# Kernel optimization log

Hardware: AMD Instinct MI355X
Metric: run time of the kernel (lower is better)

The kernel has to match this reference:

```python
import jax, jax.numpy as jnp
import numpy as np

B, L, DIM, H = 2, 2048, 2048, 16
D = DIM // H  # head_dim = 128
EPS = 1e-6


def _rope_freqs(seq_len: int, head_dim: int, theta: float = 10000.0) -> jnp.ndarray:
    # Flux-style rotation matrix: [1, 1, L, D/2, 2, 2]
    pos = np.arange(seq_len, dtype=np.float32)
    inv = 1.0 / (theta ** (np.arange(0, head_dim, 2, dtype=np.float32) / head_dim))
    ang = np.einsum('l,d->ld', pos, inv)  # [L, D/2]
    cos, sin = np.cos(ang), np.sin(ang)
    rot = np.stack([np.stack([cos, -sin], -1), np.stack([sin, cos], -1)], -2)  # [L, D/2, 2, 2]
    return jnp.asarray(rot[None, None])


def _rms_norm(x, scale):
    rrms = jax.lax.rsqrt(jnp.mean(jnp.square(x), axis=-1, keepdims=True) + EPS)
    return x * rrms * scale


def _apply_rope(xq, xk, freqs_cis):
    # xq/xk: [B, H, L, D]; freqs_cis: [1, 1, L, D/2, 2, 2]
    def rot(x):
        xr = x.reshape(*x.shape[:-1], -1, 1, 2)  # [B,H,L,D/2,1,2]
        out = freqs_cis[..., 0] * xr[..., 0] + freqs_cis[..., 1] * xr[..., 1]
        return out.reshape(x.shape)
    return rot(xq), rot(xk)


def setup_inputs() -> dict:
    key = jax.random.key(0)
    ks = jax.random.split(key, 4)
    x = jax.random.normal(ks[0], (B, L, DIM), dtype=jnp.float32)
    qkv_w = jax.random.normal(ks[1], (DIM, 3 * DIM), dtype=jnp.float32) * 0.02
    qkv_b = jnp.zeros((3 * DIM,), dtype=jnp.float32)
    q_scale = jnp.ones((D,), dtype=jnp.float32)
    k_scale = jnp.ones((D,), dtype=jnp.float32)
    proj_w = jax.random.normal(ks[2], (DIM, DIM), dtype=jnp.float32) * 0.02
    proj_b = jnp.zeros((DIM,), dtype=jnp.float32)
    pe = _rope_freqs(L, D)
    return {"x": x, "pe": pe, "qkv_w": qkv_w, "qkv_b": qkv_b,
            "q_scale": q_scale, "k_scale": k_scale,
            "proj_w": proj_w, "proj_b": proj_b}


def reference(x, pe, qkv_w, qkv_b, q_scale, k_scale, proj_w, proj_b):
    b, l, _ = x.shape
    qkv = x @ qkv_w + qkv_b                      # [B, L, 3*DIM]
    qkv = qkv.reshape(b, l, 3, H, D)
    qkv = jnp.transpose(qkv, (2, 0, 3, 1, 4))    # [3, B, H, L, D]
    q, k, v = qkv[0], qkv[1], qkv[2]
    q = _rms_norm(q, q_scale)
    k = _rms_norm(k, k_scale)
    q, k = _apply_rope(q, k, pe)
    scores = jnp.einsum('bhqd,bhkd->bhqk', q, k) / jnp.sqrt(jnp.float32(D))
    attn = jax.nn.softmax(scores, axis=-1)
    o = jnp.einsum('bhqk,bhkd->bhqd', attn, v)   # [B, H, L, D]
    o = jnp.transpose(o, (0, 2, 1, 3)).reshape(b, l, H * D)
    return o @ proj_w + proj_b
```

## Files before the change

kernel.cpp:

```cpp
#include <hip/hip_runtime.h>
#include <cstdint>
#include <cstddef>

#define BB 2
#define HB 16
#define LL 2048
#define DD 128
#define MM 4096
#define KK 2048
#define N1 6144
#define N2 2048
#define BHLD (BB*HB*LL*DD)

typedef unsigned short u16;
typedef __bf16 bf16x8 __attribute__((ext_vector_type(8)));
typedef short  s16x4  __attribute__((ext_vector_type(4)));
typedef float  f32x4  __attribute__((ext_vector_type(4)));

typedef __attribute__((address_space(1))) void* as1_ptr;
typedef __attribute__((address_space(3))) void* as3_ptr;

__device__ __forceinline__ void gload16(const void* g, void* l) {
  __builtin_amdgcn_global_load_lds((as1_ptr)g, (as3_ptr)l, 16, 0, 0);
}

__device__ __forceinline__ float bf2f(u16 u) {
  union { unsigned v; float f; } c; c.v = ((unsigned)u) << 16; return c.f;
}
__device__ __forceinline__ u16 f2bf(float f) {
  unsigned u = __builtin_bit_cast(unsigned, f);
  return (u16)((u + 0x7FFFu + ((u >> 16) & 1u)) >> 16);
}


__global__ __launch_bounds__(256) void f32_to_bf16_vec(
    const float* __restrict__ in, u16* __restrict__ out, int n4) {
  int i = blockIdx.x * 256 + threadIdx.x;
  if (i >= n4) return;
  float4 v = ((const float4*)in)[i];
  ushort4 o;
  o.x = f2bf(v.x); o.y = f2bf(v.y); o.z = f2bf(v.z); o.w = f2bf(v.w);
  ((ushort4*)out)[i] = o;
}

__global__ __launch_bounds__(256) void transpose_f32_bf16(
    const float* __restrict__ in, u16* __restrict__ out, int R, int C) {
  __shared__ float t[32][33];
  int c0 = blockIdx.x * 32, r0 = blockIdx.y * 32;
  int tx = threadIdx.x & 31, ty = threadIdx.x >> 5;
#pragma unroll
  for (int i = ty; i < 32; i += 8)
    t[i][tx] = in[(size_t)(r0 + i) * C + c0 + tx];
  __syncthreads();
#pragma unroll
  for (int i = ty; i < 32; i += 8)
    out[(size_t)(c0 + i) * R + r0 + tx] = f2bf(t[tx][i]);
}

template<int MODE>
__global__ __launch_bounds__(256, 4) void gemm_bt(
    const u16* __restrict__ A, const u16* __restrict__ Bt,
    const float* __restrict__ bias, void* __restrict__ Cout,
    const float* __restrict__ pe, const float* __restrict__ qsc,
    const float* __restrict__ ksc,
    int Msz, int Nsz, int Ksz)
{
  __shared__ __align__(16) u16 As[128*64];
  __shared__ __align__(16) u16 Bs[128*64];
  const int tid  = threadIdx.x;
  const int lane = tid & 63;
  const int wid  = tid >> 6;
  const int l15  = lane & 15, quad = lane >> 4;
  const int m0 = blockIdx.y * 128, n0 = blockIdx.x * 128;
  const int wm = (wid >> 1) * 64, wn = (wid & 1) * 64;

  f32x4 acc[4][4] = {};

  for (int ks = 0; ks < Ksz; ks += 64) {
    __syncthreads();
#pragma unroll
    for (int j = 0; j < 4; j++) {
      const int s = (wid*4 + j)*64 + lane;
      const int row = s >> 3, pc = (s & 7) ^ (row & 7);
      gload16(&A [(size_t)(m0 + row) * Ksz + ks + pc*8], &As[(wid*4 + j)*512]);
      gload16(&Bt[(size_t)(n0 + row) * Ksz + ks + pc*8], &Bs[(wid*4 + j)*512]);
    }
    __syncthreads();
#pragma unroll
    for (int kh = 0; kh < 2; kh++) {
      bf16x8 af[4], bfr[4];
#pragma unroll
      for (int i = 0; i < 4; i++) {
        const int r = wm + i*16 + l15;
        af[i]  = *(const bf16x8*)&As[r*64 + (((kh*4 + quad) ^ (r & 7)))*8];
      }
#pragma unroll
      for (int i = 0; i < 4; i++) {
        const int r = wn + i*16 + l15;
        bfr[i] = *(const bf16x8*)&Bs[r*64 + (((kh*4 + quad) ^ (r & 7)))*8];
      }
#pragma unroll
      for (int i = 0; i < 4; i++)
#pragma unroll
        for (int j = 0; j < 4; j++)
          acc[i][j] = __builtin_amdgcn_mfma_f32_16x16x32_bf16(af[i], bfr[j], acc[i][j], 0, 0, 0);
    }
  }

  if (MODE == 0) {
    u16* qkvp = (u16*)Cout;
    const int t = n0 >> 11;
    const int hh = (n0 & 2047) >> 7;
#pragma unroll
    for (int i = 0; i < 4; i++)
#pragma unroll
      for (int j = 0; j < 4; j++) {
        const float bv = bias[n0 + wn + j*16 + l15];
#pragma unroll
        for (int r = 0; r < 4; r++) acc[i][j][r] += bv;
      }

    if (t == 2) {
#pragma unroll
      for (int i = 0; i < 4; i++)
#pragma unroll
        for (int j = 0; j < 4; j++) {
          const int d = wn + j*16 + l15;
#pragma unroll
          for (int r = 0; r < 4; r++) {
            const int row = m0 + wm + i*16 + quad*4 + r;
            const int b = row >> 11, l = row & (LL - 1);
            qkvp[(size_t)2 * BHLD + (((size_t)(b*HB + hh)) * DD + d) * LL + l] =
                f2bf(acc[i][j][r]);
          }
        }
    } else {
      float (*red)[2] = (float (*)[2])As;
      const float* sc = (t == 0) ? qsc : ksc;
      __syncthreads();
#pragma unroll
      for (int i = 0; i < 4; i++)
#pragma unroll
        for (int r = 0; r < 4; r++) {
          float s2 = 0.f;
#pragma unroll
          for (int j = 0; j < 4; j++) { const float v = acc[i][j][r]; s2 += v * v; }
#pragma unroll
          for (int m = 1; m < 16; m <<= 1) s2 += __shfl_xor(s2, m, 64);
          if (l15 == 0) red[wm + i*16 + quad*4 + r][wid & 1] = s2;
        }
      __syncthreads();
#pragma unroll
      for (int i = 0; i < 4; i++)
#pragma unroll
        for (int r = 0; r < 4; r++) {
          const int rowl = wm + i*16 + quad*4 + r;
          const float tot = red[rowl][0] + red[rowl][1];
          float rr = rsqrtf(tot * (1.0f/128.0f) + 1e-6f);
          if (t == 0) rr *= 0.08838834764831845f;
          const int row = m0 + rowl, b = row >> 11, l = row & (LL - 1);
#pragma unroll
          for (int j = 0; j < 4; j++) {
            const int d = wn + j*16 + l15;
            const float y = acc[i][j][r] * rr * sc[d];
            const float p = __shfl_xor(y, 1, 64);
            const float2 pp = *(const float2*)&pe[(size_t)l * 256 + (d >> 1) * 4 + (d & 1) * 2];
            const float o = pp.x * ((d & 1) ? p : y) + pp.y * ((d & 1) ? y : p);
            qkvp[(size_t)t * BHLD + (((size_t)(b*HB + hh)) * LL + l) * DD + d] = f2bf(o);
          }
        }
    }
  } else {
#pragma unroll
    for (int i = 0; i < 4; i++)
#pragma unroll
      for (int j = 0; j < 4; j++) {
        const int col = n0 + wn + j*16 + l15;
        const float bv = bias[col];
#pragma unroll
        for (int r = 0; r < 4; r++) {
          const int row = m0 + wm + i*16 + quad*4 + r;
          ((float*)Cout)[(size_t)row * Nsz + col] = acc[i][j][r] + bv;
        }
      }
  }
}

#define BKT 64
__global__ __launch_bounds__(256, 2) void attn(
    const u16* __restrict__ qkv, u16* __restrict__ Oout)
{
  __shared__ __align__(16) u16 Ksh[2][BKT * DD];
  __shared__ __align__(16) u16 Vsh[2][DD * BKT];

  const int bh = blockIdx.x >> 4, qt = blockIdx.x & 15;
  const int wid = threadIdx.x >> 6, lane = threadIdx.x & 63;
  const int l15 = lane & 15, quad = lane >> 4;
  const int q0 = qt * 128 + wid * 32;
  const u16* qp = qkv + (size_t)bh * LL * DD;
  const u16* kp = qkv + (size_t)BHLD + (size_t)bh * LL * DD;
  const u16* vp = qkv + (size_t)2 * BHLD + (size_t)bh * DD * LL;

  bf16x8 qb[2][4];
#pragma unroll
  for (int qf = 0; qf < 2; qf++)
#pragma unroll
    for (int f = 0; f < 4; f++)
      qb[qf][f] = *(const bf16x8*)&qp[(size_t)(q0 + qf*16 + l15) * DD + f*32 + quad*8];

  float l_acc[2] = {0.f, 0.f};
  f32x4 oacc[2][8] = {};

  auto stage = [&](int buf, int k0) {
#pragma unroll
    for (int j = 0; j < 4; j++) {
      const int s = (wid*4 + j)*64 + lane;
      {
        const int r = s >> 4, c = s & 15;
        const int lc = (c & 8) | ((c & 7) ^ (r & 7));
        gload16(&kp[(size_t)(k0 + r) * DD + lc*8], &Ksh[buf][(wid*4 + j)*512]);
      }
      {
        const int r = s >> 3, c = s & 7;
        const int lc = c ^ (r & 7);
        gload16(&vp[(size_t)r * LL + k0 + lc*8], &Vsh[buf][(wid*4 + j)*512]);
      }
    }
  };

  stage(0, 0);
  int cur = 0;

  for (int k0 = 0; k0 < LL; k0 += BKT) {
    __syncthreads();
    if (k0 + BKT < LL) stage(cur ^ 1, k0 + BKT);

    f32x4 s[2][4] = {};
#pragma unroll
    for (int f = 0; f < 4; f++) {
      bf16x8 kf[4];
#pragma unroll
      for (int mt = 0; mt < 4; mt++) {
        const int rr = mt*16 + l15;
        const int Lc = f*4 + quad;
        const int pc = (Lc & 8) | ((Lc & 7) ^ (rr & 7));
        kf[mt] = *(const bf16x8*)&Ksh[cur][rr*DD + pc*8];
      }
      __builtin_amdgcn_s_setprio(1);
#pragma unroll
      for (int qf = 0; qf < 2; qf++)
#pragma unroll
        for (int mt = 0; mt < 4; mt++)
          s[qf][mt] = __builtin_amdgcn_mfma_f32_16x16x32_bf16(kf[mt], qb[qf][f], s[qf][mt], 0, 0, 0);
      __builtin_amdgcn_s_setprio(0);
    }

    s16x4 pa[2][4];
#pragma unroll
    for (int qf = 0; qf < 2; qf++) {
#pragma unroll
      for (int mt = 0; mt < 4; mt++) {
        float p0 = __expf(s[qf][mt][0] - 12.f);
        float p1 = __expf(s[qf][mt][1] - 12.f);
        float p2 = __expf(s[qf][mt][2] - 12.f);
        float p3 = __expf(s[qf][mt][3] - 12.f);
        l_acc[qf] += (p0 + p1) + (p2 + p3);
        pa[qf][mt][0] = __builtin_bit_cast(short, (__bf16)p0);
        pa[qf][mt][1] = __builtin_bit_cast(short, (__bf16)p1);
        pa[qf][mt][2] = __builtin_bit_cast(short, (__bf16)p2);
        pa[qf][mt][3] = __builtin_bit_cast(short, (__bf16)p3);
      }
    }

#pragma unroll
    for (int t = 0; t < 4; t++) {
      s16x4 vb[8];
#pragma unroll
      for (int c = 0; c < 8; c++) {
        const int rv = c*16 + l15;
        const int pc = (t*2 + (quad >> 1)) ^ (l15 & 7);
        vb[c] = *(const s16x4*)&Vsh[cur][rv*BKT + pc*8 + (quad & 1)*4];
      }
      __builtin_amdgcn_s_setprio(1);
#pragma unroll
      for (int qf = 0; qf < 2; qf++)
#pragma unroll
        for (int c = 0; c < 8; c++)
          oacc[qf][c] = __builtin_amdgcn_mfma_f32_16x16x16bf16_1k(pa[qf][t], vb[c], oacc[qf][c], 0, 0, 0);
      __builtin_amdgcn_s_setprio(0);
    }
    cur ^= 1;
  }

#pragma unroll
  for (int qf = 0; qf < 2; qf++) {
    l_acc[qf] += __shfl_xor(l_acc[qf], 16, 64);
    l_acc[qf] += __shfl_xor(l_acc[qf], 32, 64);
  }
  const int b = bh >> 4, h = bh & 15;
#pragma unroll
  for (int qf = 0; qf < 2; qf++) {
    float lr[4];
#pragma unroll
    for (int r = 0; r < 4; r++)
      lr[r] = 1.0f / __shfl(l_acc[qf], (quad << 4) | (quad*4 + r), 64);
#pragma unroll
    for (int c = 0; c < 8; c++)
#pragma unroll
      for (int r = 0; r < 4; r++) {
        int qrow = q0 + qf*16 + quad*4 + r;
        Oout[((size_t)(b*LL + qrow)) * N2 + h*DD + c*16 + l15] = f2bf(oacc[qf][c][r] * lr[r]);
      }
  }
}


extern "C" void kernel_launch(void* const* d_in, const int* in_sizes, int n_in,
                              void* d_out, int out_size, void* d_ws, size_t ws_size,
                              hipStream_t stream) {
  const float* x       = (const float*)d_in[0];
  const float* pe      = (const float*)d_in[1];
  const float* qkv_w   = (const float*)d_in[2];
  const float* qkv_b   = (const float*)d_in[3];
  const float* q_scale = (const float*)d_in[4];
  const float* k_scale = (const float*)d_in[5];
  const float* proj_w  = (const float*)d_in[6];
  const float* proj_b  = (const float*)d_in[7];

  char* ws = (char*)d_ws;
  u16* xb   = (u16*)(ws + 0);
  u16* w1t  = (u16*)(ws + 16777216);
  u16* w2t  = (u16*)(ws + 41943040);
  u16* qkv  = (u16*)(ws + 50331648);
  u16* attO = (u16*)(ws + 100663296);

  f32_to_bf16_vec<<<(MM*KK/4)/256, 256, 0, stream>>>(x, xb, MM*KK/4);
  transpose_f32_bf16<<<dim3(N1/32, KK/32), 256, 0, stream>>>(qkv_w, w1t, KK, N1);
  transpose_f32_bf16<<<dim3(N2/32, KK/32), 256, 0, stream>>>(proj_w, w2t, KK, N2);
  gemm_bt<0><<<dim3(N1/128, MM/128), 256, 0, stream>>>(
      xb, w1t, qkv_b, (void*)qkv, pe, q_scale, k_scale, MM, N1, KK);
  attn<<<BB*HB*(LL/128), 256, 0, stream>>>(qkv, attO);
  gemm_bt<1><<<dim3(N2/128, MM/128), 256, 0, stream>>>(
      attO, w2t, proj_b, d_out, nullptr, nullptr, nullptr, MM, N2, KK);
}
```

Before: 406.7 us.

## Shrink attention and proj GEMM tiles for more blocks and occupancy

Result: slower. 445.1 us (+9.4%).

```diff
diff --git a/kernel.cpp b/kernel.cpp
--- a/kernel.cpp
+++ b/kernel.cpp
@@ -45,19 +45,19 @@
 
 __global__ __launch_bounds__(256) void transpose_f32_bf16(
     const float* __restrict__ in, u16* __restrict__ out, int R, int C) {
-  __shared__ float t[32][33];
-  int c0 = blockIdx.x * 32, r0 = blockIdx.y * 32;
-  int tx = threadIdx.x & 31, ty = threadIdx.x >> 5;
-#pragma unroll
-  for (int i = ty; i < 32; i += 8)
+  __shared__ float t[64][65];
+  int c0 = blockIdx.x * 64, r0 = blockIdx.y * 64;
+  int tx = threadIdx.x & 63, ty = threadIdx.x >> 6;
+#pragma unroll
+  for (int i = ty; i < 64; i += 4)
     t[i][tx] = in[(size_t)(r0 + i) * C + c0 + tx];
   __syncthreads();
 #pragma unroll
-  for (int i = ty; i < 32; i += 8)
+  for (int i = ty; i < 64; i += 4)
     out[(size_t)(c0 + i) * R + r0 + tx] = f2bf(t[tx][i]);
 }
 
-template<int MODE>
+template<int MODE, int BN>
 __global__ __launch_bounds__(256, 4) void gemm_bt(
     const u16* __restrict__ A, const u16* __restrict__ Bt,
     const float* __restrict__ bias, void* __restrict__ Cout,
@@ -66,15 +66,17 @@
     int Msz, int Nsz, int Ksz)
 {
   __shared__ __align__(16) u16 As[128*64];
-  __shared__ __align__(16) u16 Bs[128*64];
+  __shared__ __align__(16) u16 Bs[BN*64];
   const int tid  = threadIdx.x;
   const int lane = tid & 63;
   const int wid  = tid >> 6;
   const int l15  = lane & 15, quad = lane >> 4;
-  const int m0 = blockIdx.y * 128, n0 = blockIdx.x * 128;
-  const int wm = (wid >> 1) * 64, wn = (wid & 1) * 64;
-
-  f32x4 acc[4][4] = {};
+  const int m0 = blockIdx.y * 128, n0 = blockIdx.x * BN;
+  const int wm = (BN == 128) ? (wid >> 1) * 64 : wid * 32;
+  const int wn = (BN == 128) ? (wid & 1) * 64 : 0;
+  constexpr int NI = (BN == 128) ? 4 : 2;
+
+  f32x4 acc[NI][4] = {};
 
   for (int ks = 0; ks < Ksz; ks += 64) {
     __syncthreads();
@@ -82,15 +84,24 @@
     for (int j = 0; j < 4; j++) {
       const int s = (wid*4 + j)*64 + lane;
       const int row = s >> 3, pc = (s & 7) ^ (row & 7);
-      gload16(&A [(size_t)(m0 + row) * Ksz + ks + pc*8], &As[(wid*4 + j)*512]);
-      gload16(&Bt[(size_t)(n0 + row) * Ksz + ks + pc*8], &Bs[(wid*4 + j)*512]);
+      gload16(&A[(size_t)(m0 + row) * Ksz + ks + pc*8], &As[(wid*4 + j)*512]);
+      if constexpr (BN == 128)
+        gload16(&Bt[(size_t)(n0 + row) * Ksz + ks + pc*8], &Bs[(wid*4 + j)*512]);
+    }
+    if constexpr (BN == 64) {
+#pragma unroll
+      for (int j = 0; j < 2; j++) {
+        const int s = (wid*2 + j)*64 + lane;
+        const int row = s >> 3, pc = (s & 7) ^ (row & 7);
+        gload16(&Bt[(size_t)(n0 + row) * Ksz + ks + pc*8], &Bs[(wid*2 + j)*512]);
+      }
     }
     __syncthreads();
 #pragma unroll
     for (int kh = 0; kh < 2; kh++) {
-      bf16x8 af[4], bfr[4];
-#pragma unroll
-      for (int i = 0; i < 4; i++) {
+      bf16x8 af[NI], bfr[4];
+#pragma unroll
+      for (int i = 0; i < NI; i++) {
         const int r = wm + i*16 + l15;
         af[i]  = *(const bf16x8*)&As[r*64 + (((kh*4 + quad) ^ (r & 7)))*8];
       }
@@ -100,14 +111,14 @@
         bfr[i] = *(const bf16x8*)&Bs[r*64 + (((kh*4 + quad) ^ (r & 7)))*8];
       }
 #pragma unroll
-      for (int i = 0; i < 4; i++)
+      for (int i = 0; i < NI; i++)
 #pragma unroll
         for (int j = 0; j < 4; j++)
           acc[i][j] = __builtin_amdgcn_mfma_f32_16x16x32_bf16(af[i], bfr[j], acc[i][j], 0, 0, 0);
     }
   }
 
-  if (MODE == 0) {
+  if constexpr (MODE == 0) {
     u16* qkvp = (u16*)Cout;
     const int t = n0 >> 11;
     const int hh = (n0 & 2047) >> 7;
@@ -172,7 +183,7 @@
     }
   } else {
 #pragma unroll
-    for (int i = 0; i < 4; i++)
+    for (int i = 0; i < NI; i++)
 #pragma unroll
       for (int j = 0; j < 4; j++) {
         const int col = n0 + wn + j*16 + l15;
@@ -186,44 +197,42 @@
   }
 }
 
-#define BKT 64
-__global__ __launch_bounds__(256, 2) void attn(
+#define BKT 32
+__global__ __launch_bounds__(256, 4) void attn(
     const u16* __restrict__ qkv, u16* __restrict__ Oout)
 {
   __shared__ __align__(16) u16 Ksh[2][BKT * DD];
   __shared__ __align__(16) u16 Vsh[2][DD * BKT];
 
-  const int bh = blockIdx.x >> 4, qt = blockIdx.x & 15;
+  const int bh = blockIdx.x >> 5, qt = blockIdx.x & 31;
   const int wid = threadIdx.x >> 6, lane = threadIdx.x & 63;
   const int l15 = lane & 15, quad = lane >> 4;
-  const int q0 = qt * 128 + wid * 32;
+  const int q0 = qt * 64 + wid * 16;
   const u16* qp = qkv + (size_t)bh * LL * DD;
   const u16* kp = qkv + (size_t)BHLD + (size_t)bh * LL * DD;
   const u16* vp = qkv + (size_t)2 * BHLD + (size_t)bh * DD * LL;
 
-  bf16x8 qb[2][4];
-#pragma unroll
-  for (int qf = 0; qf < 2; qf++)
-#pragma unroll
-    for (int f = 0; f < 4; f++)
-      qb[qf][f] = *(const bf16x8*)&qp[(size_t)(q0 + qf*16 + l15) * DD + f*32 + quad*8];
-
-  float l_acc[2] = {0.f, 0.f};
-  f32x4 oacc[2][8] = {};
+  bf16x8 qb[4];
+#pragma unroll
+  for (int f = 0; f < 4; f++)
+    qb[f] = *(const bf16x8*)&qp[(size_t)(q0 + l15) * DD + f*32 + quad*8];
+
+  float l_acc = 0.f;
+  f32x4 oacc[8] = {};
 
   auto stage = [&](int buf, int k0) {
 #pragma unroll
-    for (int j = 0; j < 4; j++) {
-      const int s = (wid*4 + j)*64 + lane;
+    for (int j = 0; j < 2; j++) {
+      const int s = (wid*2 + j)*64 + lane;
       {
         const int r = s >> 4, c = s & 15;
         const int lc = (c & 8) | ((c & 7) ^ (r & 7));
-        gload16(&kp[(size_t)(k0 + r) * DD + lc*8], &Ksh[buf][(wid*4 + j)*512]);
+        gload16(&kp[(size_t)(k0 + r) * DD + lc*8], &Ksh[buf][(wid*2 + j)*512]);
       }
       {
-        const int r = s >> 3, c = s & 7;
-        const int lc = c ^ (r & 7);
-        gload16(&vp[(size_t)r * LL + k0 + lc*8], &Vsh[buf][(wid*4 + j)*512]);
+        const int r = s >> 2, c = s & 3;
+        const int lc = c ^ ((r >> 1) & 3);
+        gload16(&vp[(size_t)r * LL + k0 + lc*8], &Vsh[buf][(wid*2 + j)*512]);
       }
     }
   };
@@ -235,12 +244,12 @@
     __syncthreads();
     if (k0 + BKT < LL) stage(cur ^ 1, k0 + BKT);
 
-    f32x4 s[2][4] = {};
+    f32x4 s[2] = {};
 #pragma unroll
     for (int f = 0; f < 4; f++) {
-      bf16x8 kf[4];
-#pragma unroll
-      for (int mt = 0; mt < 4; mt++) {
+      bf16x8 kf[2];
+#pragma unroll
+      for (int mt = 0; mt < 2; mt++) {
         const int rr = mt*16 + l15;
         const int Lc = f*4 + quad;
         const int pc = (Lc & 8) | ((Lc & 7) ^ (rr & 7));
@@ -248,70 +257,57 @@
       }
       __builtin_amdgcn_s_setprio(1);
 #pragma unroll
-      for (int qf = 0; qf < 2; qf++)
-#pragma unroll
-        for (int mt = 0; mt < 4; mt++)
-          s[qf][mt] = __builtin_amdgcn_mfma_f32_16x16x32_bf16(kf[mt], qb[qf][f], s[qf][mt], 0, 0, 0);
+      for (int mt = 0; mt < 2; mt++)
+        s[mt] = __builtin_amdgcn_mfma_f32_16x16x32_bf16(kf[mt], qb[f], s[mt], 0, 0, 0);
       __builtin_amdgcn_s_setprio(0);
     }
 
-    s16x4 pa[2][4];
-#pragma unroll
-    for (int qf = 0; qf < 2; qf++) {
-#pragma unroll
-      for (int mt = 0; mt < 4; mt++) {
-        float p0 = __expf(s[qf][mt][0] - 12.f);
-        float p1 = __expf(s[qf][mt][1] - 12.f);
-        float p2 = __expf(s[qf][mt][2] - 12.f);
-        float p3 = __expf(s[qf][mt][3] - 12.f);
-        l_acc[qf] += (p0 + p1) + (p2 + p3);
-        pa[qf][mt][0] = __builtin_bit_cast(short, (__bf16)p0);
-        pa[qf][mt][1] = __builtin_bit_cast(short, (__bf16)p1);
-        pa[qf][mt][2] = __builtin_bit_cast(short, (__bf16)p2);
-        pa[qf][mt][3] = __builtin_bit_cast(short, (__bf16)p3);
-      }
-    }
-
-#pragma unroll
-    for (int t = 0; t < 4; t++) {
+    s16x4 pa[2];
+#pragma unroll
+    for (int mt = 0; mt < 2; mt++) {
+      float p0 = __expf(s[mt][0] - 12.f);
+      float p1 = __expf(s[mt][1] - 12.f);
+      float p2 = __expf(s[mt][2] - 12.f);
+      float p3 = __expf(s[mt][3] - 12.f);
+      l_acc += (p0 + p1) + (p2 + p3);
+      pa[mt][0] = __builtin_bit_cast(short, (__bf16)p0);
+      pa[mt][1] = __builtin_bit_cast(short, (__bf16)p1);
+      pa[mt][2] = __builtin_bit_cast(short, (__bf16)p2);
+      pa[mt][3] = __builtin_bit_cast(short, (__bf16)p3);
+    }
+
+#pragma unroll
+    for (int t = 0; t < 2; t++) {
       s16x4 vb[8];
 #pragma unroll
       for (int c = 0; c < 8; c++) {
         const int rv = c*16 + l15;
-        const int pc = (t*2 + (quad >> 1)) ^ (l15 & 7);
+        const int pc = (t*2 + (quad >> 1)) ^ ((rv >> 1) & 3);
         vb[c] = *(const s16x4*)&Vsh[cur][rv*BKT + pc*8 + (quad & 1)*4];
       }
       __builtin_amdgcn_s_setprio(1);
 #pragma unroll
-      for (int qf = 0; qf < 2; qf++)
-#pragma unroll
-        for (int c = 0; c < 8; c++)
-          oacc[qf][c] = __builtin_amdgcn_mfma_f32_16x16x16bf16_1k(pa[qf][t], vb[c], oacc[qf][c], 0, 0, 0);
+      for (int c = 0; c < 8; c++)
+        oacc[c] = __builtin_amdgcn_mfma_f32_16x16x16bf16_1k(pa[t], vb[c], oacc[c], 0, 0, 0);
       __builtin_amdgcn_s_setprio(0);
     }
     cur ^= 1;
   }
 
-#pragma unroll
-  for (int qf = 0; qf < 2; qf++) {
-    l_acc[qf] += __shfl_xor(l_acc[qf], 16, 64);
-    l_acc[qf] += __shfl_xor(l_acc[qf], 32, 64);
-  }
+  l_acc += __shfl_xor(l_acc, 16, 64);
+  l_acc += __shfl_xor(l_acc, 32, 64);
   const int b = bh >> 4, h = bh & 15;
-#pragma unroll
-  for (int qf = 0; qf < 2; qf++) {
-    float lr[4];
-#pragma unroll
-    for (int r = 0; r < 4; r++)
-      lr[r] = 1.0f / __shfl(l_acc[qf], (quad << 4) | (quad*4 + r), 64);
-#pragma unroll
-    for (int c = 0; c < 8; c++)
-#pragma unroll
-      for (int r = 0; r < 4; r++) {
-        int qrow = q0 + qf*16 + quad*4 + r;
-        Oout[((size_t)(b*LL + qrow)) * N2 + h*DD + c*16 + l15] = f2bf(oacc[qf][c][r] * lr[r]);
-      }
-  }
+  float lr[4];
+#pragma unroll
+  for (int r = 0; r < 4; r++)
+    lr[r] = 1.0f / __shfl(l_acc, (quad << 4) | (quad*4 + r), 64);
+#pragma unroll
+  for (int c = 0; c < 8; c++)
+#pragma unroll
+    for (int r = 0; r < 4; r++) {
+      int qrow = q0 + quad*4 + r;
+      Oout[((size_t)(b*LL + qrow)) * N2 + h*DD + c*16 + l15] = f2bf(oacc[c][r] * lr[r]);
+    }
 }
 
 
@@ -335,11 +331,11 @@
   u16* attO = (u16*)(ws + 100663296);
 
   f32_to_bf16_vec<<<(MM*KK/4)/256, 256, 0, stream>>>(x, xb, MM*KK/4);
-  transpose_f32_bf16<<<dim3(N1/32, KK/32), 256, 0, stream>>>(qkv_w, w1t, KK, N1);
-  transpose_f32_bf16<<<dim3(N2/32, KK/32), 256, 0, stream>>>(proj_w, w2t, KK, N2);
-  gemm_bt<0><<<dim3(N1/128, MM/128), 256, 0, stream>>>(
+  transpose_f32_bf16<<<dim3(N1/64, KK/64), 256, 0, stream>>>(qkv_w, w1t, KK, N1);
+  transpose_f32_bf16<<<dim3(N2/64, KK/64), 256, 0, stream>>>(proj_w, w2t, KK, N2);
+  gemm_bt<0,128><<<dim3(N1/128, MM/128), 256, 0, stream>>>(
       xb, w1t, qkv_b, (void*)qkv, pe, q_scale, k_scale, MM, N1, KK);
-  attn<<<BB*HB*(LL/128), 256, 0, stream>>>(qkv, attO);
-  gemm_bt<1><<<dim3(N2/128, MM/128), 256, 0, stream>>>(
+  attn<<<BB*HB*(LL/64), 256, 0, stream>>>(qkv, attO);
+  gemm_bt<1,64><<<dim3(N2/64, MM/128), 256, 0, stream>>>(
       attO, w2t, proj_b, d_out, nullptr, nullptr, nullptr, MM, N2, KK);
 }
```
